# Kernel optimization log

Hardware: AMD Instinct MI355X
Metric: run time of the kernel (lower is better)

The kernel has to match this reference:

```python
import jax, jax.numpy as jnp
import numpy as np
from jax import lax

N_T, B, C_IN, H, W = 24, 2, 9, 32, 32   # n timesteps, batch, bands, tile HxW
N_FILTER, KM, N_CLASS, HID = 32, 16, 10, 128


def setup_inputs() -> dict:
    key = jax.random.key(0)
    ks = jax.random.split(key, 6)
    x = jax.random.normal(ks[0], (N_T, B, C_IN, H, W), jnp.float32)
    kernels = jax.random.normal(ks[1], (N_FILTER, KM, C_IN), jnp.float32)  # DTW filter kernels
    W1 = jax.random.normal(ks[2], (N_FILTER, HID), jnp.float32) * 0.1
    b1 = jnp.zeros((HID,), jnp.float32)
    W2 = jax.random.normal(ks[3], (HID, HID), jnp.float32) * 0.1
    b2 = jnp.zeros((HID,), jnp.float32)
    Wl = jax.random.normal(ks[4], (HID, N_CLASS), jnp.float32) * 0.1
    bl = jnp.zeros((N_CLASS,), jnp.float32)
    return {"x": x, "kernels": kernels, "W1": W1, "b1": b1, "W2": W2, "b2": b2, "Wl": Wl, "bl": bl}


def _dtw_single(kernel, seq):
    # kernel: (m, c), seq: (n, c). Classic DTW with squared-euclidean local cost,
    # then sum of local costs along the optimal alignment path (path is non-diff,
    # matching the torch code's detached dtw_path + differentiable squared diffs).
    C = jnp.sum((kernel[:, None, :] - seq[None, :, :]) ** 2, axis=-1)  # (m, n)
    m, n = C.shape
    inf = jnp.array(jnp.inf, C.dtype)
    row0 = jnp.cumsum(C[0])

    def row_step(prev, crow):
        prev_shift = jnp.concatenate([jnp.full((1,), inf, C.dtype), prev[:-1]])
        def col_step(left, cud):
            c, up, diag = cud
            d = c + jnp.minimum(left, jnp.minimum(up, diag))
            return d, d
        _, row = lax.scan(col_step, inf, (crow, prev, prev_shift))
        return row, row

    _, rows = lax.scan(row_step, row0, C[1:])
    D = lax.stop_gradient(jnp.concatenate([row0[None, :], rows], axis=0))  # (m, n)

    def bt_step(carry, _):
        i, j, acc, done = carry
        im1 = jnp.maximum(i - 1, 0)
        jm1 = jnp.maximum(j - 1, 0)
        cand = jnp.stack([
            jnp.where((i > 0) & (j > 0), D[im1, jm1], inf),  # diagonal
            jnp.where(i > 0, D[im1, j], inf),                # up
            jnp.where(j > 0, D[i, jm1], inf)])               # left
        choice = jnp.argmin(cand)  # first-min tie-break = diagonal preferred (as np.argmin)
        ni = jnp.where(choice == 2, i, im1)
        nj = jnp.where(choice == 1, j, jm1)
        ni = jnp.where(done, i, ni)
        nj = jnp.where(done, j, nj)
        acc = acc + jnp.where(done, jnp.array(0.0, C.dtype), C[ni, nj])
        done = done | ((ni == 0) & (nj == 0))
        return (ni, nj, acc, done), None

    init = (jnp.int32(m - 1), jnp.int32(n - 1), C[m - 1, n - 1], jnp.array(m == 1 and n == 1))
    (_, _, total, _), _ = lax.scan(bt_step, init, None, length=m + n - 2)
    return total


def reference(x, kernels, W1, b1, W2, b2, Wl, bl):
    n, b, c, h, w = x.shape
    # torch.cat(list_of_n, dim=0).view(-1, n, c) == row-major reshape of (n,b,c,h,w)
    seqs = x.reshape(-1, n, c)  # (B2, n, c), B2 = b*h*w
    feats = jax.vmap(lambda s: jax.vmap(lambda k: _dtw_single(k, s))(kernels))(seqs)  # (B2, F)
    t = jax.nn.relu(feats @ W1 + b1)
    t = jax.nn.relu(t @ W2 + b2)
    t = jax.nn.softmax(t @ Wl + bl, axis=1)
    return t.reshape(b, N_CLASS, h, w)
```

## Files before the change

kernel.cpp:

```cpp
#include <hip/hip_runtime.h>

#define NT   24
#define CIN  9
#define NF   32
#define KM   16
#define HID  128
#define NCLS 10
#define SEQ_LEN (NT*CIN)
#define PADJ 12
#define NSTRIP 4

__global__ __launch_bounds__(128, 4) void dtwnet_fused(
    const float* __restrict__ x,
    const float* __restrict__ kern,
    const float* __restrict__ W1, const float* __restrict__ b1,
    const float* __restrict__ W2, const float* __restrict__ b2,
    const float* __restrict__ Wl, const float* __restrict__ bl,
    float* __restrict__ out)
{
  __shared__ float seq_lds[NT*PADJ];
  __shared__ float bcol[NT];
  __shared__ float feat_lds[NF];
  __shared__ float h1_lds[HID];
  __shared__ float h2_lds[HID];
  __shared__ float logit_lds[NCLS];

  const int tid  = threadIdx.x;
  const int bid  = blockIdx.x;
  const int wave = tid >> 6;
  const int lane = tid & 63;
  const int s    = lane >> 4;
  const int f_lo = lane & 15;
  const int f    = wave*16 + f_lo;

  float kf[4*CIN];
  {
    const float4* kp = (const float4*)(kern + f*(KM*CIN) + s*(4*CIN));
    float4 t0 = kp[0], t1 = kp[1], t2 = kp[2], t3 = kp[3], t4 = kp[4],
           t5 = kp[5], t6 = kp[6], t7 = kp[7], t8 = kp[8];
    kf[0]=t0.x; kf[1]=t0.y; kf[2]=t0.z; kf[3]=t0.w;
    kf[4]=t1.x; kf[5]=t1.y; kf[6]=t1.z; kf[7]=t1.w;
    kf[8]=t2.x; kf[9]=t2.y; kf[10]=t2.z; kf[11]=t2.w;
    kf[12]=t3.x; kf[13]=t3.y; kf[14]=t3.z; kf[15]=t3.w;
    kf[16]=t4.x; kf[17]=t4.y; kf[18]=t4.z; kf[19]=t4.w;
    kf[20]=t5.x; kf[21]=t5.y; kf[22]=t5.z; kf[23]=t5.w;
    kf[24]=t6.x; kf[25]=t6.y; kf[26]=t6.z; kf[27]=t6.w;
    kf[28]=t7.x; kf[29]=t7.y; kf[30]=t7.z; kf[31]=t7.w;
    kf[32]=t8.x; kf[33]=t8.y; kf[34]=t8.z; kf[35]=t8.w;
  }

  for (int d = tid; d < SEQ_LEN; d += 128) {
    int jj = d / CIN, cc = d - jj*CIN;
    seq_lds[jj*PADJ + cc] = x[bid*SEQ_LEN + d];
  }
  __syncthreads();

  if (tid < NT) {
    const float4* sp = (const float4*)(seq_lds + tid*PADJ);
    float4 q0 = sp[0], q1 = sp[1], q2 = sp[2];
    float b = q0.x*q0.x + q0.y*q0.y + q0.z*q0.z + q0.w*q0.w
            + q1.x*q1.x + q1.y*q1.y + q1.z*q1.z + q1.w*q1.w
            + q2.x*q2.x;
    bcol[tid] = b;
  }

  float arow[4];
  #pragma unroll
  for (int r = 0; r < 4; ++r) {
    float a = 0.f;
    #pragma unroll
    for (int c = 0; c < CIN; ++c) a = fmaf(kf[r*CIN+c], kf[r*CIN+c], a);
    arow[r] = a;
  }
  #pragma unroll
  for (int q = 0; q < 4*CIN; ++q) kf[q] *= -2.f;
  __syncthreads();

  float rowD[4];
  float bndUp = 0.f, bndDg = 0.f;

  #pragma unroll 1
  for (int t = 0; t < NT + NSTRIP - 1; ++t) {
    int j = t - s;
    bool active = (j >= 0) && (j < NT);
    float nb = 0.f;
    if (active) {
      const float4* sp = (const float4*)(seq_lds + j*PADJ);
      float4 q0 = sp[0], q1 = sp[1], q2 = sp[2];
      float bj = bcol[j];
      float sv[CIN] = {q0.x,q0.y,q0.z,q0.w,q1.x,q1.y,q1.z,q1.w,q2.x};
      float cost[4];
      #pragma unroll
      for (int r = 0; r < 4; ++r) {
        float cc = arow[r] + bj;
        #pragma unroll
        for (int c = 0; c < CIN; ++c) cc = fmaf(kf[r*CIN+c], sv[c], cc);
        cost[r] = cc;
      }
      if (j == 0) {
        float acc = (s == 0) ? 0.f : bndUp;
        #pragma unroll
        for (int r = 0; r < 4; ++r) { acc += cost[r]; rowD[r] = acc; }
      } else {
        float up, diag;
        float left = rowD[0];
        float D0;
        if (s == 0) {
          D0 = cost[0] + left;
        } else {
          D0 = cost[0] + fminf(bndDg, fminf(bndUp, left));
        }
        diag = left;
        rowD[0] = D0; up = D0;
        #pragma unroll
        for (int r = 1; r < 4; ++r) {
          float lD = rowD[r];
          float D2 = cost[r] + fminf(diag, fminf(up, lD));
          diag = lD;
          rowD[r] = D2; up = D2;
        }
      }
      nb = rowD[3];
    }
    float rD = __shfl_up(nb, 16u);
    bndDg = bndUp;
    bndUp = rD;
  }

  if (s == 3) feat_lds[f] = rowD[3];
  __syncthreads();

  {
    float acc = b1[tid];
    #pragma unroll
    for (int k = 0; k < NF; ++k) acc = fmaf(feat_lds[k], W1[k*HID + tid], acc);
    h1_lds[tid] = fmaxf(acc, 0.f);
  }
  __syncthreads();
  {
    const float4* hh = (const float4*)h1_lds;
    float a0 = b2[tid], a1 = 0.f, a2 = 0.f, a3 = 0.f;
    #pragma unroll
    for (int k = 0; k < HID/4; ++k) {
      float4 h4 = hh[k];
      a0 = fmaf(h4.x, W2[(4*k+0)*HID + tid], a0);
      a1 = fmaf(h4.y, W2[(4*k+1)*HID + tid], a1);
      a2 = fmaf(h4.z, W2[(4*k+2)*HID + tid], a2);
      a3 = fmaf(h4.w, W2[(4*k+3)*HID + tid], a3);
    }
    h2_lds[tid] = fmaxf((a0 + a1) + (a2 + a3), 0.f);
  }
  __syncthreads();
  if (tid < NCLS) {
    const float4* hh = (const float4*)h2_lds;
    float a0 = bl[tid], a1 = 0.f, a2 = 0.f, a3 = 0.f;
    #pragma unroll
    for (int k = 0; k < HID/4; ++k) {
      float4 h4 = hh[k];
      a0 = fmaf(h4.x, Wl[(4*k+0)*NCLS + tid], a0);
      a1 = fmaf(h4.y, Wl[(4*k+1)*NCLS + tid], a1);
      a2 = fmaf(h4.z, Wl[(4*k+2)*NCLS + tid], a2);
      a3 = fmaf(h4.w, Wl[(4*k+3)*NCLS + tid], a3);
    }
    logit_lds[tid] = (a0 + a1) + (a2 + a3);
  }
  __syncthreads();
  if (tid == 0) {
    float mx = logit_lds[0];
    #pragma unroll
    for (int j = 1; j < NCLS; ++j) mx = fmaxf(mx, logit_lds[j]);
    float e[NCLS]; float sum = 0.f;
    #pragma unroll
    for (int j = 0; j < NCLS; ++j) { e[j] = __expf(logit_lds[j] - mx); sum += e[j]; }
    float inv = 1.f / sum;
    float* op = out + bid*NCLS;
    #pragma unroll
    for (int j = 0; j < NCLS; ++j) op[j] = e[j] * inv;
  }
}

extern "C" void kernel_launch(void* const* d_in, const int* in_sizes, int n_in,
                              void* d_out, int out_size, void* d_ws, size_t ws_size,
                              hipStream_t stream) {
  const float* x    = (const float*)d_in[0];
  const float* kern = (const float*)d_in[1];
  const float* W1   = (const float*)d_in[2];
  const float* b1   = (const float*)d_in[3];
  const float* W2   = (const float*)d_in[4];
  const float* b2   = (const float*)d_in[5];
  const float* Wl   = (const float*)d_in[6];
  const float* bl   = (const float*)d_in[7];
  float* out = (float*)d_out;

  dtwnet_fused<<<2048, 128, 0, stream>>>(x, kern, W1, b1, W2, b2, Wl, bl, out);
}
```

Measured before the change: 84.00 us.

## Split DTW rows into eight strips of two rows across 256 threads

Re-partitions the per-pixel DTW wavefront so each filter is handled by 8 lanes owning 2 kernel rows each instead of 4 lanes owning 4 rows. Block size doubles to 256 threads, and the MLP stages are guarded to the first 128 threads. This shortens the serial per-step dependency chain and lowers register pressure. In exchange, the wavefront takes more steps (31 vs 27), more lanes idle during the MLP tail, and there are more shuffles per block.

```diff
diff --git a/kernel.cpp b/kernel.cpp
--- a/kernel.cpp
+++ b/kernel.cpp
@@ -8,9 +8,10 @@
 #define NCLS 10
 #define SEQ_LEN (NT*CIN)
 #define PADJ 12
-#define NSTRIP 4
+#define NSTRIP 8
+#define RSTRIP 2
 
-__global__ __launch_bounds__(128, 4) void dtwnet_fused(
+__global__ __launch_bounds__(256, 8) void dtwnet_fused(
     const float* __restrict__ x,
     const float* __restrict__ kern,
     const float* __restrict__ W1, const float* __restrict__ b1,
@@ -29,27 +30,23 @@
   const int bid  = blockIdx.x;
   const int wave = tid >> 6;
   const int lane = tid & 63;
-  const int s    = lane >> 4;
-  const int f_lo = lane & 15;
-  const int f    = wave*16 + f_lo;
+  const int s    = lane >> 3;
+  const int f_lo = lane & 7;
+  const int f    = wave*8 + f_lo;
 
-  float kf[4*CIN];
+  float kf[RSTRIP*CIN];
   {
-    const float4* kp = (const float4*)(kern + f*(KM*CIN) + s*(4*CIN));
-    float4 t0 = kp[0], t1 = kp[1], t2 = kp[2], t3 = kp[3], t4 = kp[4],
-           t5 = kp[5], t6 = kp[6], t7 = kp[7], t8 = kp[8];
-    kf[0]=t0.x; kf[1]=t0.y; kf[2]=t0.z; kf[3]=t0.w;
-    kf[4]=t1.x; kf[5]=t1.y; kf[6]=t1.z; kf[7]=t1.w;
-    kf[8]=t2.x; kf[9]=t2.y; kf[10]=t2.z; kf[11]=t2.w;
-    kf[12]=t3.x; kf[13]=t3.y; kf[14]=t3.z; kf[15]=t3.w;
-    kf[16]=t4.x; kf[17]=t4.y; kf[18]=t4.z; kf[19]=t4.w;
-    kf[20]=t5.x; kf[21]=t5.y; kf[22]=t5.z; kf[23]=t5.w;
-    kf[24]=t6.x; kf[25]=t6.y; kf[26]=t6.z; kf[27]=t6.w;
-    kf[28]=t7.x; kf[29]=t7.y; kf[30]=t7.z; kf[31]=t7.w;
-    kf[32]=t8.x; kf[33]=t8.y; kf[34]=t8.z; kf[35]=t8.w;
+    const float2* kp = (const float2*)(kern + f*(KM*CIN) + s*(RSTRIP*CIN));
+    float2 t0=kp[0], t1=kp[1], t2=kp[2], t3=kp[3], t4=kp[4],
+           t5=kp[5], t6=kp[6], t7=kp[7], t8=kp[8];
+    kf[0]=t0.x; kf[1]=t0.y; kf[2]=t1.x; kf[3]=t1.y;
+    kf[4]=t2.x; kf[5]=t2.y; kf[6]=t3.x; kf[7]=t3.y;
+    kf[8]=t4.x; kf[9]=t4.y; kf[10]=t5.x; kf[11]=t5.y;
+    kf[12]=t6.x; kf[13]=t6.y; kf[14]=t7.x; kf[15]=t7.y;
+    kf[16]=t8.x; kf[17]=t8.y;
   }
 
-  for (int d = tid; d < SEQ_LEN; d += 128) {
+  for (int d = tid; d < SEQ_LEN; d += 256) {
     int jj = d / CIN, cc = d - jj*CIN;
     seq_lds[jj*PADJ + cc] = x[bid*SEQ_LEN + d];
   }
@@ -58,25 +55,24 @@
   if (tid < NT) {
     const float4* sp = (const float4*)(seq_lds + tid*PADJ);
     float4 q0 = sp[0], q1 = sp[1], q2 = sp[2];
-    float b = q0.x*q0.x + q0.y*q0.y + q0.z*q0.z + q0.w*q0.w
-            + q1.x*q1.x + q1.y*q1.y + q1.z*q1.z + q1.w*q1.w
-            + q2.x*q2.x;
-    bcol[tid] = b;
+    bcol[tid] = q0.x*q0.x + q0.y*q0.y + q0.z*q0.z + q0.w*q0.w
+              + q1.x*q1.x + q1.y*q1.y + q1.z*q1.z + q1.w*q1.w
+              + q2.x*q2.x;
   }
 
-  float arow[4];
+  float arow[RSTRIP];
   #pragma unroll
-  for (int r = 0; r < 4; ++r) {
+  for (int r = 0; r < RSTRIP; ++r) {
     float a = 0.f;
     #pragma unroll
     for (int c = 0; c < CIN; ++c) a = fmaf(kf[r*CIN+c], kf[r*CIN+c], a);
     arow[r] = a;
   }
   #pragma unroll
-  for (int q = 0; q < 4*CIN; ++q) kf[q] *= -2.f;
+  for (int q = 0; q < RSTRIP*CIN; ++q) kf[q] *= -2.f;
   __syncthreads();
 
-  float rowD[4];
+  float rowD[RSTRIP];
   float bndUp = 0.f, bndDg = 0.f;
 
   #pragma unroll 1
@@ -89,55 +85,46 @@
       float4 q0 = sp[0], q1 = sp[1], q2 = sp[2];
       float bj = bcol[j];
       float sv[CIN] = {q0.x,q0.y,q0.z,q0.w,q1.x,q1.y,q1.z,q1.w,q2.x};
-      float cost[4];
+      float c0 = arow[0] + bj, c1 = arow[1] + bj;
       #pragma unroll
-      for (int r = 0; r < 4; ++r) {
-        float cc = arow[r] + bj;
-        #pragma unroll
-        for (int c = 0; c < CIN; ++c) cc = fmaf(kf[r*CIN+c], sv[c], cc);
-        cost[r] = cc;
+      for (int c = 0; c < CIN; ++c) {
+        c0 = fmaf(kf[c], sv[c], c0);
+        c1 = fmaf(kf[CIN+c], sv[c], c1);
       }
       if (j == 0) {
         float acc = (s == 0) ? 0.f : bndUp;
-        #pragma unroll
-        for (int r = 0; r < 4; ++r) { acc += cost[r]; rowD[r] = acc; }
+        acc += c0; rowD[0] = acc;
+        acc += c1; rowD[1] = acc;
       } else {
-        float up, diag;
         float left = rowD[0];
         float D0;
         if (s == 0) {
-          D0 = cost[0] + left;
+          D0 = c0 + left;
         } else {
-          D0 = cost[0] + fminf(bndDg, fminf(bndUp, left));
+          D0 = c0 + fminf(bndDg, fminf(bndUp, left));
         }
-        diag = left;
-        rowD[0] = D0; up = D0;
-        #pragma unroll
-        for (int r = 1; r < 4; ++r) {
-          float lD = rowD[r];
-          float D2 = cost[r] + fminf(diag, fminf(up, lD));
-          diag = lD;
-          rowD[r] = D2; up = D2;
-        }
+        float lD = rowD[1];
+        float D1 = c1 + fminf(left, fminf(D0, lD));
+        rowD[0] = D0; rowD[1] = D1;
       }
-      nb = rowD[3];
+      nb = rowD[1];
     }
-    float rD = __shfl_up(nb, 16u);
+    float rD = __shfl_up(nb, 8u);
     bndDg = bndUp;
     bndUp = rD;
   }
 
-  if (s == 3) feat_lds[f] = rowD[3];
+  if (s == NSTRIP-1) feat_lds[f] = rowD[1];
   __syncthreads();
 
-  {
+  if (tid < HID) {
     float acc = b1[tid];
     #pragma unroll
     for (int k = 0; k < NF; ++k) acc = fmaf(feat_lds[k], W1[k*HID + tid], acc);
     h1_lds[tid] = fmaxf(acc, 0.f);
   }
   __syncthreads();
-  {
+  if (tid < HID) {
     const float4* hh = (const float4*)h1_lds;
     float a0 = b2[tid], a1 = 0.f, a2 = 0.f, a3 = 0.f;
     #pragma unroll
@@ -192,5 +179,5 @@
   const float* bl   = (const float*)d_in[7];
   float* out = (float*)d_out;
 
-  dtwnet_fused<<<2048, 128, 0, stream>>>(x, kern, W1, b1, W2, b2, Wl, bl, out);
+  dtwnet_fused<<<2048, 256, 0, stream>>>(x, kern, W1, b1, W2, b2, Wl, bl, out);
 }
```

New measurement: 87.89 us. 1.05x slower.
